# Kernel optimization log

Hardware: AMD Instinct MI355X
Metric: run time of the kernel (lower is better)

## Reference

```python
import jax, jax.numpy as jnp
import numpy as np

DIM = 128      # d_model (C)
DEPTH = 8
D_INNER = 2 * DIM      # expand=2
D_STATE = 16
D_CONV = 4
DT_RANK = (DIM + 15) // 16  # ceil(d_model/16) = 8
EPS = 1e-6
B_SZ, H_SZ, W_SZ = 2, 64, 64


def setup_inputs() -> dict:
    key = jax.random.key(0)
    ks = jax.random.split(key, 8)
    s = 0.02
    f32 = jnp.float32
    inp = {
        "x": jax.random.normal(ks[0], (B_SZ, DIM, H_SZ, W_SZ), f32),
        "in_proj_w": (jax.random.normal(ks[1], (DEPTH, 2 * D_INNER, DIM), f32) * s),
        "conv_w": (jax.random.normal(ks[2], (DEPTH, D_INNER, D_CONV), f32) * s),
        "conv_b": jnp.zeros((DEPTH, D_INNER), f32),
        "x_proj_w": (jax.random.normal(ks[3], (DEPTH, DT_RANK + 2 * D_STATE, D_INNER), f32) * s),
        "dt_proj_w": (jax.random.normal(ks[4], (DEPTH, D_INNER, DT_RANK), f32) * s),
        "dt_proj_b": jax.random.uniform(ks[5], (DEPTH, D_INNER), f32, -4.0, -2.0),
        "A_log": jnp.tile(jnp.log(jnp.arange(1.0, D_STATE + 1.0, dtype=f32))[None, None, :], (DEPTH, D_INNER, 1)),
        "D_skip": jnp.ones((DEPTH, D_INNER), f32),
        "out_proj_w": (jax.random.normal(ks[6], (DEPTH, DIM, D_INNER), f32) * s),
        "rms_w": jnp.ones((DIM,), f32),
    }
    return inp


def _selective_scan(u, delta, A, Bm, Cm, D_skip):
    # u, delta: [B,L,Dn]; A: [Dn,N]; Bm, Cm: [B,L,N]; D_skip: [Dn]
    dA = jnp.exp(delta[..., None] * A)                      # [B,L,Dn,N]
    dBu = (delta * u)[..., None] * Bm[:, :, None, :]        # [B,L,Dn,N]
    def comb(c1, c2):
        a1, b1 = c1
        a2, b2 = c2
        return a1 * a2, a2 * b1 + b2
    _, h = jax.lax.associative_scan(comb, (dA, dBu), axis=1)  # h: [B,L,Dn,N]
    y = jnp.einsum('bldn,bln->bld', h, Cm) + u * D_skip
    return y


def _mamba_layer(x, in_w, cw, cb, xp_w, dtw, dtb, A_log, D_skip, out_w):
    # x: [B,L,D]
    xz = jnp.einsum('bld,ed->ble', x, in_w)                 # [B,L,2*Dn]
    xin, z = jnp.split(xz, 2, axis=-1)
    # causal depthwise conv1d, kernel D_CONV, left-pad D_CONV-1
    lhs = jnp.transpose(xin, (0, 2, 1))                     # [B,Dn,L]
    rhs = cw[:, None, :]                                    # [Dn,1,K]
    xc = jax.lax.conv_general_dilated(
        lhs, rhs, window_strides=(1,), padding=[(D_CONV - 1, 0)],
        dimension_numbers=('NCH', 'OIH', 'NCH'), feature_group_count=D_INNER)
    xc = xc + cb[None, :, None]
    xc = jax.nn.silu(jnp.transpose(xc, (0, 2, 1)))          # [B,L,Dn]
    x_dbl = jnp.einsum('bld,ed->ble', xc, xp_w)             # [B,L,dt_rank+2N]
    dt, Bm, Cm = jnp.split(x_dbl, [DT_RANK, DT_RANK + D_STATE], axis=-1)
    delta = jax.nn.softplus(jnp.einsum('blr,dr->bld', dt, dtw) + dtb)
    A = -jnp.exp(A_log)                                     # [Dn,N]
    y = _selective_scan(xc, delta, A, Bm, Cm, D_skip)       # [B,L,Dn]
    y = y * jax.nn.silu(z)
    return jnp.einsum('bld,od->blo', y, out_w)              # [B,L,D]


def reference(x, in_proj_w, conv_w, conv_b, x_proj_w, dt_proj_w, dt_proj_b,
              A_log, D_skip, out_proj_w, rms_w):
    B, C, H, W = x.shape
    h = jnp.transpose(x.reshape(B, C, H * W), (0, 2, 1))    # [B,L,C]
    for i in range(DEPTH):
        h = _mamba_layer(h, in_proj_w[i], conv_w[i], conv_b[i], x_proj_w[i],
                         dt_proj_w[i], dt_proj_b[i], A_log[i], D_skip[i],
                         out_proj_w[i])
    # RMSNorm over channel dim
    h = h * jax.lax.rsqrt(jnp.mean(h * h, axis=-1, keepdims=True) + EPS) * rms_w
    return jnp.transpose(h.reshape(B, H, W, C), (0, 3, 1, 2))
```

## Files before the change

kernel.cpp:

```cpp
#include <hip/hip_runtime.h>
#include <math.h>

#define B_SZ   2
#define L_SEQ  4096
#define DIMC   128
#define DI     256
#define DST    16
#define DTR    8
#define NXP    40
#define NXPP   48
#define NLAYER 8
#define NCH    256
#define CS     16
#define LOG2E  1.4426950408889634f
#define LN2    0.6931471805599453f
#define PSA    264

#define N_INW  (NLAYER * 512 * 128)
#define N_XPW  (NLAYER * NXPP * DI)
#define N_OW   (NLAYER * DIMC * DI)
#define N_AF   (NLAYER * DI * DST)

typedef __attribute__((ext_vector_type(8))) unsigned short u16x8;
typedef __attribute__((ext_vector_type(4))) float f32x4;

__device__ __forceinline__ float fexp2(float x){ float r; asm("v_exp_f32 %0, %1" : "=v"(r) : "v"(x)); return r; }
__device__ __forceinline__ float flog2(float x){ float r; asm("v_log_f32 %0, %1" : "=v"(r) : "v"(x)); return r; }
__device__ __forceinline__ float frcp (float x){ float r; asm("v_rcp_f32 %0, %1" : "=v"(r) : "v"(x)); return r; }

__device__ __forceinline__ float silu_f(float x) {
    return x * frcp(1.f + fexp2(-x * LOG2E));
}
__device__ __forceinline__ float softplus_f(float x) {
    float t = fexp2(-fabsf(x) * LOG2E);
    return fmaxf(x, 0.f) + flog2(1.f + t) * LN2;
}
__device__ __forceinline__ void splitf(float x, unsigned short& h, unsigned short& l) {
    unsigned bx = __builtin_bit_cast(unsigned, x);
    h = (unsigned short)(bx >> 16);
    float fh = __builtin_bit_cast(float, bx & 0xffff0000u);
    float r = x - fh;
    l = (unsigned short)(__builtin_bit_cast(unsigned, r) >> 16);
}
__device__ __forceinline__ float bf2f(unsigned short u) {
    return __builtin_bit_cast(float, (unsigned)u << 16);
}

__global__ void prep(const float* __restrict__ in_w, const float* __restrict__ xp_w,
                     const float* __restrict__ out_w, const float* __restrict__ A_log,
                     unsigned short* __restrict__ iwh, unsigned short* __restrict__ iwl,
                     unsigned short* __restrict__ xpwh, unsigned short* __restrict__ xpwl,
                     unsigned short* __restrict__ owh, unsigned short* __restrict__ owl,
                     float* __restrict__ Af) {
    const int i = blockIdx.x * 256 + threadIdx.x;
    if (i < N_INW) { unsigned short h, l; splitf(in_w[i], h, l); iwh[i] = h; iwl[i] = l; }
    if (i < N_XPW) {
        int ly = i / (NXPP * DI), rem = i % (NXPP * DI);
        int c = rem / DI, k = rem % DI;
        unsigned short h = 0, l = 0;
        if (c < NXP) splitf(xp_w[((size_t)ly * NXP + c) * DI + k], h, l);
        xpwh[i] = h; xpwl[i] = l;
    }
    if (i < N_OW) { unsigned short h, l; splitf(out_w[i], h, l); owh[i] = h; owl[i] = l; }
    if (i < N_AF) Af[i] = -expf(A_log[i]) * LOG2E;
}

__global__ void transpose_in(const float* __restrict__ x, unsigned short* __restrict__ hh,
                             unsigned short* __restrict__ hl) {
    __shared__ float tl[32][33];
    const int b  = blockIdx.x;
    const int c0 = blockIdx.y * 32;
    const int l0 = blockIdx.z * 32;
    const int tx = threadIdx.x;
    const int ty = threadIdx.y;
    #pragma unroll
    for (int r = 0; r < 4; ++r) {
        int c = c0 + ty + r * 8;
        tl[ty + r * 8][tx] = x[((size_t)b * DIMC + c) * L_SEQ + l0 + tx];
    }
    __syncthreads();
    #pragma unroll
    for (int r = 0; r < 4; ++r) {
        int l = l0 + ty + r * 8;
        float v = tl[tx][ty + r * 8];
        size_t o = ((size_t)b * L_SEQ + l) * DIMC + c0 + tx;
        unsigned short h16, l16; splitf(v, h16, l16);
        hh[o] = h16; hl[o] = l16;
    }
}

template<int BM, int BN>
__global__ __launch_bounds__(256) void gemm_sp(
    const unsigned short* __restrict__ Ahg, const unsigned short* __restrict__ Alg,
    const unsigned short* __restrict__ Whg, const unsigned short* __restrict__ Wlg,
    float* __restrict__ C, int M, int N, int K) {
    constexpr int PS = 40;
    __shared__ unsigned short lds[(BM + BN) * 2 * PS];
    unsigned short* LAh = lds;
    unsigned short* LAl = LAh + BM * PS;
    unsigned short* LBh = LAl + BM * PS;
    unsigned short* LBl = LBh + BN * PS;
    const int t = threadIdx.x;
    const int w = t >> 6, l = t & 63;
    const int wr = w >> 1, wc = w & 1;
    const int lr = l & 15, lq = l >> 4;
    constexpr int MF = BM / 32, NF = BN / 32;
    const int bm = blockIdx.x * BM, bn = blockIdx.y * BN;
    f32x4 acc[MF][NF];
    const f32x4 z4 = {0.f, 0.f, 0.f, 0.f};
    #pragma unroll
    for (int m = 0; m < MF; ++m)
        #pragma unroll
        for (int n = 0; n < NF; ++n) acc[m][n] = z4;

    for (int k0 = 0; k0 < K; k0 += 32) {
        if (k0) __syncthreads();
        #pragma unroll
        for (int s = 0; s < BM * 4 / 256; ++s) {
            int task = t + s * 256;
            int r = task >> 2, g = task & 3;
            size_t go = (size_t)(bm + r) * K + k0 + g * 8;
            *(u16x8*)&LAh[r * PS + g * 8] = *(const u16x8*)&Ahg[go];
            *(u16x8*)&LAl[r * PS + g * 8] = *(const u16x8*)&Alg[go];
        }
        #pragma unroll
        for (int s = 0; s < BN * 4 / 256; ++s) {
            int task = t + s * 256;
            int r = task >> 2, g = task & 3;
            size_t go = (size_t)(bn + r) * K + k0 + g * 8;
            *(u16x8*)&LBh[r * PS + g * 8] = *(const u16x8*)&Whg[go];
            *(u16x8*)&LBl[r * PS + g * 8] = *(const u16x8*)&Wlg[go];
        }
        __syncthreads();
        u16x8 ah[MF], al[MF], bh[NF], bl[NF];
        #pragma unroll
        for (int m = 0; m < MF; ++m) {
            int rr = wr * (BM / 2) + m * 16 + lr;
            ah[m] = *(u16x8*)&LAh[rr * PS + lq * 8];
            al[m] = *(u16x8*)&LAl[rr * PS + lq * 8];
        }
        #pragma unroll
        for (int n = 0; n < NF; ++n) {
            int rr = wc * (BN / 2) + n * 16 + lr;
            bh[n] = *(u16x8*)&LBh[rr * PS + lq * 8];
            bl[n] = *(u16x8*)&LBl[rr * PS + lq * 8];
        }
        #pragma unroll
        for (int m = 0; m < MF; ++m)
            #pragma unroll
            for (int n = 0; n < NF; ++n) {
                asm("v_mfma_f32_16x16x32_bf16 %0, %1, %2, %0" : "+v"(acc[m][n]) : "v"(ah[m]), "v"(bh[n]));
                asm("v_mfma_f32_16x16x32_bf16 %0, %1, %2, %0" : "+v"(acc[m][n]) : "v"(ah[m]), "v"(bl[n]));
                asm("v_mfma_f32_16x16x32_bf16 %0, %1, %2, %0" : "+v"(acc[m][n]) : "v"(al[m]), "v"(bh[n]));
            }
    }
    #pragma unroll
    for (int m = 0; m < MF; ++m)
        #pragma unroll
        for (int n = 0; n < NF; ++n) {
            int col = bn + wc * (BN / 2) + n * 16 + lr;
            #pragma unroll
            for (int r = 0; r < 4; ++r) {
                int row = bm + wr * (BM / 2) + m * 16 + lq * 4 + r;
                C[(size_t)row * N + col] = acc[m][n][r];
            }
        }
}

__global__ __launch_bounds__(256) void fused_mid(
    const float* __restrict__ xz,
    const unsigned short* __restrict__ xpwh, const unsigned short* __restrict__ xpwl,
    const float* __restrict__ dtw, const float* __restrict__ dtb,
    const float* __restrict__ cw, const float* __restrict__ cb,
    const float* __restrict__ Af_g,
    float* __restrict__ xdbl, float* __restrict__ paO, float* __restrict__ hO) {
    const int ch = blockIdx.x & (NCH - 1);
    const int d  = threadIdx.x;
    const size_t r0 = (size_t)(blockIdx.x >> 8) * L_SEQ + ch * CS;
    __shared__ unsigned short aS[2][CS][PSA];
    __shared__ float P[4][CS][49];
    __shared__ float xdblS[CS][41];

    {
        const float w0 = cw[d * 4 + 0], w1 = cw[d * 4 + 1];
        const float w2 = cw[d * 4 + 2], w3 = cw[d * 4 + 3];
        const float bz = cb[d];
        float p0 = 0.f, p1 = 0.f, p2 = 0.f;
        if (ch > 0) {
            p0 = xz[(r0 - 3) * 512 + d];
            p1 = xz[(r0 - 2) * 512 + d];
            p2 = xz[(r0 - 1) * 512 + d];
        }
        #pragma unroll 4
        for (int i = 0; i < CS; ++i) {
            float cur = xz[(r0 + i) * 512 + d];
            float v = silu_f(fmaf(w3, cur, fmaf(w2, p2, fmaf(w1, p1, fmaf(w0, p0, bz)))));
            unsigned short h16, l16; splitf(v, h16, l16);
            aS[0][i][d] = h16; aS[1][i][d] = l16;
            p0 = p1; p1 = p2; p2 = cur;
        }
    }
    __syncthreads();

    const int w = threadIdx.x >> 6, l = threadIdx.x & 63;
    const int lr = l & 15, lq = l >> 4;
    {
        f32x4 acc[3];
        const f32x4 z4 = {0.f, 0.f, 0.f, 0.f};
        #pragma unroll
        for (int n = 0; n < 3; ++n) acc[n] = z4;
        #pragma unroll
        for (int ks = 0; ks < 2; ++ks) {
            const int kk = w * 64 + ks * 32 + lq * 8;
            u16x8 ah, al, bh[3], bl[3];
            ah = *(const u16x8*)&aS[0][lr][kk];
            al = *(const u16x8*)&aS[1][lr][kk];
            #pragma unroll
            for (int n = 0; n < 3; ++n) {
                const int c = n * 16 + lr;
                bh[n] = *(const u16x8*)&xpwh[c * DI + kk];
                bl[n] = *(const u16x8*)&xpwl[c * DI + kk];
            }
            #pragma unroll
            for (int n = 0; n < 3; ++n) {
                asm("v_mfma_f32_16x16x32_bf16 %0, %1, %2, %0" : "+v"(acc[n]) : "v"(ah), "v"(bh[n]));
                asm("v_mfma_f32_16x16x32_bf16 %0, %1, %2, %0" : "+v"(acc[n]) : "v"(ah), "v"(bl[n]));
                asm("v_mfma_f32_16x16x32_bf16 %0, %1, %2, %0" : "+v"(acc[n]) : "v"(al), "v"(bh[n]));
            }
        }
        #pragma unroll
        for (int n = 0; n < 3; ++n)
            #pragma unroll
            for (int r = 0; r < 4; ++r)
                P[w][lq * 4 + r][n * 16 + lr] = acc[n][r];
    }
    __syncthreads();
    {
        const int i = threadIdx.x >> 4;
        const int cb0 = threadIdx.x & 15;
        for (int c = cb0; c < NXP; c += 16) {
            float s = P[0][i][c] + P[1][i][c] + P[2][i][c] + P[3][i][c];
            xdblS[i][c] = s;
            xdbl[(r0 + i) * NXP + c] = s;
        }
    }
    __syncthreads();

    float wt[DTR];
    #pragma unroll
    for (int r = 0; r < DTR; ++r) wt[r] = dtw[d * DTR + r];
    const float bt = dtb[d];
    float Af[DST], h[DST], pa[DST];
    #pragma unroll
    for (int n = 0; n < DST; ++n) {
        Af[n] = Af_g[d * DST + n];
        h[n] = 0.f; pa[n] = 1.f;
    }
    #pragma unroll 4
    for (int i = 0; i < CS; ++i) {
        float s = bt;
        #pragma unroll
        for (int r = 0; r < DTR; ++r) s = fmaf(xdblS[i][r], wt[r], s);
        const float dl = softplus_f(s);
        const float u = bf2f(aS[0][i][d]) + bf2f(aS[1][i][d]);
        const float du = dl * u;
        #pragma unroll
        for (int n = 0; n < DST; ++n) {
            const float dA = fexp2(dl * Af[n]);
            pa[n] *= dA;
            h[n] = fmaf(dA, h[n], du * xdblS[i][DTR + n]);
        }
    }
    const size_t o = ((size_t)blockIdx.x * DI + d) * DST;
    #pragma unroll
    for (int n = 0; n < DST; ++n) { paO[o + n] = pa[n]; hO[o + n] = h[n]; }
}

__global__ void scan_combine(float* __restrict__ paO, const float* __restrict__ hO) {
    const int t  = blockIdx.x * 64 + threadIdx.x;
    const int b  = t / (DI * DST);
    const int dn = t % (DI * DST);
    float run = 0.f;
    for (int ch0 = 0; ch0 < NCH; ch0 += 8) {
        float pav[8], hv[8];
        #pragma unroll
        for (int j = 0; j < 8; ++j) {
            size_t o = ((size_t)(b * NCH + ch0 + j)) * DI * DST + dn;
            pav[j] = paO[o]; hv[j] = hO[o];
        }
        #pragma unroll
        for (int j = 0; j < 8; ++j) {
            size_t o = ((size_t)(b * NCH + ch0 + j)) * DI * DST + dn;
            paO[o] = run;
            run = fmaf(pav[j], run, hv[j]);
        }
    }
}

__global__ __launch_bounds__(256) void fused_out(
    const float* __restrict__ xz, const float* __restrict__ xdbl,
    const unsigned short* __restrict__ owh, const unsigned short* __restrict__ owl,
    const float* __restrict__ dtw, const float* __restrict__ dtb,
    const float* __restrict__ cw, const float* __restrict__ cb,
    const float* __restrict__ Af_g, const float* __restrict__ D_skip,
    const float* __restrict__ hinit,
    unsigned short* __restrict__ hh, unsigned short* __restrict__ hl) {
    const int ch = blockIdx.x & (NCH - 1);
    const int d  = threadIdx.x;
    const size_t r0 = (size_t)(blockIdx.x >> 8) * L_SEQ + ch * CS;
    __shared__ unsigned short yS[2][CS][PSA];
    __shared__ float xdblS[CS][41];

    {
        const float* src = xdbl + r0 * NXP;
        for (int idx = threadIdx.x; idx < CS * NXP; idx += 256)
            xdblS[idx / NXP][idx % NXP] = src[idx];
    }
    float wt[DTR];
    #pragma unroll
    for (int r = 0; r < DTR; ++r) wt[r] = dtw[d * DTR + r];
    const float bt = dtb[d];
    const float Dd = D_skip[d];
    const float w0 = cw[d * 4 + 0], w1 = cw[d * 4 + 1];
    const float w2 = cw[d * 4 + 2], w3 = cw[d * 4 + 3];
    const float bz = cb[d];
    float Af[DST], h[DST];
    const size_t o = ((size_t)blockIdx.x * DI + d) * DST;
    #pragma unroll
    for (int n = 0; n < DST; ++n) {
        Af[n] = Af_g[d * DST + n];
        h[n] = hinit[o + n];
    }
    float p0 = 0.f, p1 = 0.f, p2 = 0.f;
    if (ch > 0) {
        p0 = xz[(r0 - 3) * 512 + d];
        p1 = xz[(r0 - 2) * 512 + d];
        p2 = xz[(r0 - 1) * 512 + d];
    }
    __syncthreads();

    #pragma unroll 4
    for (int i = 0; i < CS; ++i) {
        const float cur = xz[(r0 + i) * 512 + d];
        const float zv  = xz[(r0 + i) * 512 + DI + d];
        const float u = silu_f(fmaf(w3, cur, fmaf(w2, p2, fmaf(w1, p1, fmaf(w0, p0, bz)))));
        p0 = p1; p1 = p2; p2 = cur;
        float s = bt;
        #pragma unroll
        for (int r = 0; r < DTR; ++r) s = fmaf(xdblS[i][r], wt[r], s);
        const float dl = softplus_f(s);
        const float du = dl * u;
        float acc = 0.f;
        #pragma unroll
        for (int n = 0; n < DST; ++n) {
            const float dA = fexp2(dl * Af[n]);
            h[n] = fmaf(dA, h[n], du * xdblS[i][DTR + n]);
            acc = fmaf(h[n], xdblS[i][DTR + DST + n], acc);
        }
        const float y = (acc + u * Dd) * silu_f(zv);
        unsigned short h16, l16; splitf(y, h16, l16);
        yS[0][i][d] = h16; yS[1][i][d] = l16;
    }
    __syncthreads();

    const int w = threadIdx.x >> 6, l = threadIdx.x & 63;
    const int lr = l & 15, lq = l >> 4;
    f32x4 acc[2];
    const f32x4 z4 = {0.f, 0.f, 0.f, 0.f};
    #pragma unroll
    for (int n = 0; n < 2; ++n) acc[n] = z4;
    #pragma unroll
    for (int ks = 0; ks < 8; ++ks) {
        const int kk = ks * 32 + lq * 8;
        u16x8 ah, al, bh[2], bl[2];
        ah = *(const u16x8*)&yS[0][lr][kk];
        al = *(const u16x8*)&yS[1][lr][kk];
        #pragma unroll
        for (int n = 0; n < 2; ++n) {
            const int c = w * 32 + n * 16 + lr;
            bh[n] = *(const u16x8*)&owh[c * DI + kk];
            bl[n] = *(const u16x8*)&owl[c * DI + kk];
        }
        #pragma unroll
        for (int n = 0; n < 2; ++n) {
            asm("v_mfma_f32_16x16x32_bf16 %0, %1, %2, %0" : "+v"(acc[n]) : "v"(ah), "v"(bh[n]));
            asm("v_mfma_f32_16x16x32_bf16 %0, %1, %2, %0" : "+v"(acc[n]) : "v"(ah), "v"(bl[n]));
            asm("v_mfma_f32_16x16x32_bf16 %0, %1, %2, %0" : "+v"(acc[n]) : "v"(al), "v"(bh[n]));
        }
    }
    #pragma unroll
    for (int n = 0; n < 2; ++n) {
        const int col = w * 32 + n * 16 + lr;
        #pragma unroll
        for (int r = 0; r < 4; ++r) {
            const size_t row = r0 + lq * 4 + r;
            unsigned short h16, l16; splitf(acc[n][r], h16, l16);
            hh[row * DIMC + col] = h16;
            hl[row * DIMC + col] = l16;
        }
    }
}

__global__ void rms_out(const unsigned short* __restrict__ hh, const unsigned short* __restrict__ hl,
                        const float* __restrict__ rw, float* __restrict__ out) {
    __shared__ float tile[64][129];
    __shared__ float rinv[64];
    const int blk = blockIdx.x;
    const int b = blk / (L_SEQ / 64);
    const int l0 = (blk % (L_SEQ / 64)) * 64;
    const int t = threadIdx.x;
    for (int k = 0; k < 32; ++k) {
        int idx = k * 256 + t;
        int l = idx >> 7, cc = idx & 127;
        size_t o = ((size_t)b * L_SEQ + l0 + l) * DIMC + cc;
        tile[l][cc] = bf2f(hh[o]) + bf2f(hl[o]);
    }
    __syncthreads();
    if (t < 64) {
        float s = 0.f;
        for (int cc = 0; cc < DIMC; ++cc) { float v = tile[t][cc]; s += v * v; }
        rinv[t] = rsqrtf(s / DIMC + 1e-6f);
    }
    __syncthreads();
    for (int k = 0; k < 32; ++k) {
        int odx = k * 256 + t;
        int cc = odx >> 6, li = odx & 63;
        out[((size_t)b * DIMC + cc) * L_SEQ + l0 + li] = tile[li][cc] * rinv[li] * rw[cc];
    }
}

extern "C" void kernel_launch(void* const* d_in, const int* in_sizes, int n_in,
                              void* d_out, int out_size, void* d_ws, size_t ws_size,
                              hipStream_t stream) {
    const float* x      = (const float*)d_in[0];
    const float* in_w   = (const float*)d_in[1];
    const float* conv_w = (const float*)d_in[2];
    const float* conv_b = (const float*)d_in[3];
    const float* xp_w   = (const float*)d_in[4];
    const float* dt_w   = (const float*)d_in[5];
    const float* dt_b   = (const float*)d_in[6];
    const float* A_log  = (const float*)d_in[7];
    const float* D_skip = (const float*)d_in[8];
    const float* out_w  = (const float*)d_in[9];
    const float* rms_w  = (const float*)d_in[10];
    float* out = (float*)d_out;

    const int M = B_SZ * L_SEQ;
    char* p = (char*)d_ws;
    auto alloc = [&](size_t bytes) -> void* {
        void* r = (void*)p; p += (bytes + 255) & ~(size_t)255; return r;
    };
    float* xz   = (float*)alloc((size_t)M * 512 * 4);
    float* xdbl = (float*)alloc((size_t)M * NXP * 4);
    float* paB  = (float*)alloc((size_t)B_SZ * NCH * DI * DST * 4);
    float* hB   = (float*)alloc((size_t)B_SZ * NCH * DI * DST * 4);
    float* AfT  = (float*)alloc((size_t)N_AF * 4);
    unsigned short* hh0 = (unsigned short*)alloc((size_t)M * DIMC * 2);
    unsigned short* hl0 = (unsigned short*)alloc((size_t)M * DIMC * 2);
    unsigned short* hh1 = (unsigned short*)alloc((size_t)M * DIMC * 2);
    unsigned short* hl1 = (unsigned short*)alloc((size_t)M * DIMC * 2);
    unsigned short* iwh = (unsigned short*)alloc((size_t)N_INW * 2);
    unsigned short* iwl = (unsigned short*)alloc((size_t)N_INW * 2);
    unsigned short* xpwh = (unsigned short*)alloc((size_t)N_XPW * 2);
    unsigned short* xpwl = (unsigned short*)alloc((size_t)N_XPW * 2);
    unsigned short* owh = (unsigned short*)alloc((size_t)N_OW * 2);
    unsigned short* owl = (unsigned short*)alloc((size_t)N_OW * 2);

    prep<<<(N_INW + 255) / 256, 256, 0, stream>>>(
        in_w, xp_w, out_w, A_log, iwh, iwl, xpwh, xpwl, owh, owl, AfT);

    transpose_in<<<dim3(B_SZ, DIMC / 32, L_SEQ / 32), dim3(32, 8), 0, stream>>>(x, hh0, hl0);

    unsigned short *hhin = hh0, *hlin = hl0, *hhout = hh1, *hlout = hl1;
    for (int layer = 0; layer < NLAYER; ++layer) {
        const float* cw  = conv_w + (size_t)layer * DI * 4;
        const float* cb  = conv_b + (size_t)layer * DI;
        const float* dtw = dt_w   + (size_t)layer * DI * DTR;
        const float* dtb = dt_b   + (size_t)layer * DI;
        const float* af  = AfT    + (size_t)layer * DI * DST;
        const float* ds  = D_skip + (size_t)layer * DI;
        const size_t iwo = (size_t)layer * 512 * 128;
        const size_t xpo = (size_t)layer * NXPP * DI;
        const size_t owo = (size_t)layer * DIMC * DI;

        gemm_sp<64, 128><<<dim3(M / 64, 4), 256, 0, stream>>>(
            hhin, hlin, iwh + iwo, iwl + iwo, xz, M, 512, 128);
        fused_mid<<<B_SZ * NCH, 256, 0, stream>>>(
            xz, xpwh + xpo, xpwl + xpo, dtw, dtb, cw, cb, af, xdbl, paB, hB);
        scan_combine<<<(B_SZ * DI * DST) / 64, 64, 0, stream>>>(paB, hB);
        fused_out<<<B_SZ * NCH, 256, 0, stream>>>(
            xz, xdbl, owh + owo, owl + owo, dtw, dtb, cw, cb, af, ds, paB,
            hhout, hlout);

        unsigned short* ts;
        ts = hhin; hhin = hhout; hhout = ts;
        ts = hlin; hlin = hlout; hlout = ts;
    }

    rms_out<<<B_SZ * (L_SEQ / 64), 256, 0, stream>>>(hhin, hlin, rms_w, out);
}
```

Before: 552.9 us.

## Fuse next layer's in_proj GEMM into out_proj kernel epilogue

The out_proj result for each 16-row chunk now stays in shared memory as a bf16 hi/lo split, and the same block immediately multiplies it by the next layer's in_proj weights, writing xz for the next layer directly. This removes the separate gemm_sp launch per layer and the global round-trip of the hidden state between layers. Only the first layer's in_proj stays a standalone GEMM. The cost is an extra shared buffer, 8 accumulators per thread, and in_proj weights re-read from global by every block with small M tiles (16 rows), which may reduce MFMA efficiency compared with the dedicated GEMM.

```diff
diff --git a/kernel.cpp b/kernel.cpp
--- a/kernel.cpp
+++ b/kernel.cpp
@@ -15,6 +15,7 @@
 #define LOG2E  1.4426950408889634f
 #define LN2    0.6931471805599453f
 #define PSA    264
+#define PSH    136
 
 #define N_INW  (NLAYER * 512 * 128)
 #define N_XPW  (NLAYER * NXPP * DI)
@@ -297,18 +298,22 @@
     }
 }
 
-__global__ __launch_bounds__(256) void fused_out(
+template<int LAST>
+__global__ __launch_bounds__(256) void fused_outin(
     const float* __restrict__ xz, const float* __restrict__ xdbl,
     const unsigned short* __restrict__ owh, const unsigned short* __restrict__ owl,
+    const unsigned short* __restrict__ iwh, const unsigned short* __restrict__ iwl,
     const float* __restrict__ dtw, const float* __restrict__ dtb,
     const float* __restrict__ cw, const float* __restrict__ cb,
     const float* __restrict__ Af_g, const float* __restrict__ D_skip,
     const float* __restrict__ hinit,
-    unsigned short* __restrict__ hh, unsigned short* __restrict__ hl) {
+    float* __restrict__ xz_next,
+    unsigned short* __restrict__ hho, unsigned short* __restrict__ hlo) {
     const int ch = blockIdx.x & (NCH - 1);
     const int d  = threadIdx.x;
     const size_t r0 = (size_t)(blockIdx.x >> 8) * L_SEQ + ch * CS;
     __shared__ unsigned short yS[2][CS][PSA];
+    __shared__ unsigned short hpS[2][CS][PSH];
     __shared__ float xdblS[CS][41];
 
     {
@@ -365,27 +370,23 @@
 
     const int w = threadIdx.x >> 6, l = threadIdx.x & 63;
     const int lr = l & 15, lq = l >> 4;
+    const f32x4 z4 = {0.f, 0.f, 0.f, 0.f};
     f32x4 acc[2];
-    const f32x4 z4 = {0.f, 0.f, 0.f, 0.f};
     #pragma unroll
     for (int n = 0; n < 2; ++n) acc[n] = z4;
     #pragma unroll
     for (int ks = 0; ks < 8; ++ks) {
         const int kk = ks * 32 + lq * 8;
-        u16x8 ah, al, bh[2], bl[2];
-        ah = *(const u16x8*)&yS[0][lr][kk];
-        al = *(const u16x8*)&yS[1][lr][kk];
+        u16x8 ah = *(const u16x8*)&yS[0][lr][kk];
+        u16x8 al = *(const u16x8*)&yS[1][lr][kk];
         #pragma unroll
         for (int n = 0; n < 2; ++n) {
             const int c = w * 32 + n * 16 + lr;
-            bh[n] = *(const u16x8*)&owh[c * DI + kk];
-            bl[n] = *(const u16x8*)&owl[c * DI + kk];
-        }
-        #pragma unroll
-        for (int n = 0; n < 2; ++n) {
-            asm("v_mfma_f32_16x16x32_bf16 %0, %1, %2, %0" : "+v"(acc[n]) : "v"(ah), "v"(bh[n]));
-            asm("v_mfma_f32_16x16x32_bf16 %0, %1, %2, %0" : "+v"(acc[n]) : "v"(ah), "v"(bl[n]));
-            asm("v_mfma_f32_16x16x32_bf16 %0, %1, %2, %0" : "+v"(acc[n]) : "v"(al), "v"(bh[n]));
+            u16x8 bh = *(const u16x8*)&owh[c * DI + kk];
+            u16x8 bl = *(const u16x8*)&owl[c * DI + kk];
+            asm("v_mfma_f32_16x16x32_bf16 %0, %1, %2, %0" : "+v"(acc[n]) : "v"(ah), "v"(bh));
+            asm("v_mfma_f32_16x16x32_bf16 %0, %1, %2, %0" : "+v"(acc[n]) : "v"(ah), "v"(bl));
+            asm("v_mfma_f32_16x16x32_bf16 %0, %1, %2, %0" : "+v"(acc[n]) : "v"(al), "v"(bh));
         }
     }
     #pragma unroll
@@ -393,10 +394,43 @@
         const int col = w * 32 + n * 16 + lr;
         #pragma unroll
         for (int r = 0; r < 4; ++r) {
-            const size_t row = r0 + lq * 4 + r;
+            const int row = lq * 4 + r;
             unsigned short h16, l16; splitf(acc[n][r], h16, l16);
-            hh[row * DIMC + col] = h16;
-            hl[row * DIMC + col] = l16;
+            hpS[0][row][col] = h16; hpS[1][row][col] = l16;
+            if constexpr (LAST) {
+                hho[(r0 + row) * DIMC + col] = h16;
+                hlo[(r0 + row) * DIMC + col] = l16;
+            }
+        }
+    }
+
+    if constexpr (!LAST) {
+        __syncthreads();
+        f32x4 a2[8];
+        #pragma unroll
+        for (int n = 0; n < 8; ++n) a2[n] = z4;
+        #pragma unroll
+        for (int k0 = 0; k0 < 128; k0 += 32) {
+            u16x8 ah = *(const u16x8*)&hpS[0][lr][k0 + lq * 8];
+            u16x8 al = *(const u16x8*)&hpS[1][lr][k0 + lq * 8];
+            #pragma unroll
+            for (int n = 0; n < 8; ++n) {
+                const int col = w * 128 + n * 16 + lr;
+                u16x8 bh = *(const u16x8*)&iwh[(size_t)col * 128 + k0 + lq * 8];
+                u16x8 bl = *(const u16x8*)&iwl[(size_t)col * 128 + k0 + lq * 8];
+                asm("v_mfma_f32_16x16x32_bf16 %0, %1, %2, %0" : "+v"(a2[n]) : "v"(ah), "v"(bh));
+                asm("v_mfma_f32_16x16x32_bf16 %0, %1, %2, %0" : "+v"(a2[n]) : "v"(ah), "v"(bl));
+                asm("v_mfma_f32_16x16x32_bf16 %0, %1, %2, %0" : "+v"(a2[n]) : "v"(al), "v"(bh));
+            }
+        }
+        #pragma unroll
+        for (int n = 0; n < 8; ++n) {
+            const int col = w * 128 + n * 16 + lr;
+            #pragma unroll
+            for (int r = 0; r < 4; ++r) {
+                const size_t row = r0 + lq * 4 + r;
+                xz_next[row * 512 + col] = a2[n][r];
+            }
         }
     }
 }
@@ -450,7 +484,8 @@
     auto alloc = [&](size_t bytes) -> void* {
         void* r = (void*)p; p += (bytes + 255) & ~(size_t)255; return r;
     };
-    float* xz   = (float*)alloc((size_t)M * 512 * 4);
+    float* xzA  = (float*)alloc((size_t)M * 512 * 4);
+    float* xzB  = (float*)alloc((size_t)M * 512 * 4);
     float* xdbl = (float*)alloc((size_t)M * NXP * 4);
     float* paB  = (float*)alloc((size_t)B_SZ * NCH * DI * DST * 4);
     float* hB   = (float*)alloc((size_t)B_SZ * NCH * DI * DST * 4);
@@ -471,7 +506,10 @@
 
     transpose_in<<<dim3(B_SZ, DIMC / 32, L_SEQ / 32), dim3(32, 8), 0, stream>>>(x, hh0, hl0);
 
-    unsigned short *hhin = hh0, *hlin = hl0, *hhout = hh1, *hlout = hl1;
+    gemm_sp<64, 128><<<dim3(M / 64, 4), 256, 0, stream>>>(
+        hh0, hl0, iwh, iwl, xzA, M, 512, 128);
+
+    float *xzc = xzA, *xzn = xzB;
     for (int layer = 0; layer < NLAYER; ++layer) {
         const float* cw  = conv_w + (size_t)layer * DI * 4;
         const float* cb  = conv_b + (size_t)layer * DI;
@@ -479,23 +517,24 @@
         const float* dtb = dt_b   + (size_t)layer * DI;
         const float* af  = AfT    + (size_t)layer * DI * DST;
         const float* ds  = D_skip + (size_t)layer * DI;
-        const size_t iwo = (size_t)layer * 512 * 128;
         const size_t xpo = (size_t)layer * NXPP * DI;
         const size_t owo = (size_t)layer * DIMC * DI;
-
-        gemm_sp<64, 128><<<dim3(M / 64, 4), 256, 0, stream>>>(
-            hhin, hlin, iwh + iwo, iwl + iwo, xz, M, 512, 128);
+        const size_t iwo_next = (size_t)(layer + 1) * 512 * 128;
+
         fused_mid<<<B_SZ * NCH, 256, 0, stream>>>(
-            xz, xpwh + xpo, xpwl + xpo, dtw, dtb, cw, cb, af, xdbl, paB, hB);
+            xzc, xpwh + xpo, xpwl + xpo, dtw, dtb, cw, cb, af, xdbl, paB, hB);
         scan_combine<<<(B_SZ * DI * DST) / 64, 64, 0, stream>>>(paB, hB);
-        fused_out<<<B_SZ * NCH, 256, 0, stream>>>(
-            xz, xdbl, owh + owo, owl + owo, dtw, dtb, cw, cb, af, ds, paB,
-            hhout, hlout);
-
-        unsigned short* ts;
-        ts = hhin; hhin = hhout; hhout = ts;
-        ts = hlin; hlin = hlout; hlout = ts;
-    }
-
-    rms_out<<<B_SZ * (L_SEQ / 64), 256, 0, stream>>>(hhin, hlin, rms_w, out);
-}
+        if (layer < NLAYER - 1) {
+            fused_outin<0><<<B_SZ * NCH, 256, 0, stream>>>(
+                xzc, xdbl, owh + owo, owl + owo, iwh + iwo_next, iwl + iwo_next,
+                dtw, dtb, cw, cb, af, ds, paB, xzn, nullptr, nullptr);
+        } else {
+            fused_outin<1><<<B_SZ * NCH, 256, 0, stream>>>(
+                xzc, xdbl, owh + owo, owl + owo, nullptr, nullptr,
+                dtw, dtb, cw, cb, af, ds, paB, nullptr, hh1, hl1);
+        }
+        float* tf = xzc; xzc = xzn; xzn = tf;
+    }
+
+    rms_out<<<B_SZ * (L_SEQ / 64), 256, 0, stream>>>(hh1, hl1, rms_w, out);
+}
```

Result: slower. 566.3 us (+2.4%).
